# Optimization experiments

Hardware: AMD Instinct MI355X
Metric: run time of the kernel (lower is better)

## Reference

```python
import jax, jax.numpy as jnp
import numpy as np

N, D, H, E = 32768, 1024, 1024, 4


def setup_inputs() -> dict:
    key = jax.random.key(0)
    ks = jax.random.split(key, 10)
    s = 0.02  # xavier-ish init scale for stability
    return {
        "features": jax.random.normal(ks[0], (N, D), dtype=jnp.float32),
        "symbol_ids": jax.random.randint(ks[1], (N,), 0, E, dtype=jnp.int32),
        "W1": jax.random.normal(ks[2], (E, D, H), dtype=jnp.float32) * s,
        "b1": jax.random.normal(ks[3], (E, H), dtype=jnp.float32) * s,
        "W2": jax.random.normal(ks[4], (E, H, H), dtype=jnp.float32) * s,
        "b2": jax.random.normal(ks[5], (E, H), dtype=jnp.float32) * s,
        "W3": jax.random.normal(ks[6], (E, H, 1), dtype=jnp.float32) * s,
        "b3": jax.random.normal(ks[7], (E, 1), dtype=jnp.float32) * s,
        "slope": jax.random.normal(ks[8], (E,), dtype=jnp.float32),
        "intercept": jax.random.normal(ks[9], (E,), dtype=jnp.float32),
    }


def reference(features, symbol_ids, W1, b1, W2, b2, W3, b3, slope, intercept):
    # Run every atom through every expert MLP (E is tiny), then select by symbol.
    # h1: [E, N, H]
    h = jax.nn.relu(jnp.einsum("nd,edh->enh", features, W1) + b1[:, None, :])
    h = jax.nn.relu(jnp.einsum("enh,ehk->enk", h, W2) + b2[:, None, :])
    y = (jnp.einsum("enk,eko->eno", h, W3) + b3[:, None, :])[..., 0]  # [E, N]
    per_atom = slope[:, None] * y + intercept[:, None]                # [E, N]
    sel = symbol_ids[None, :] == jnp.arange(E, dtype=symbol_ids.dtype)[:, None]
    atomic_energies = jnp.sum(jnp.where(sel, per_atom, 0.0), axis=0)  # [N]
    image_energy = jnp.sum(atomic_energies)                           # scalar
    return image_energy
```

## Files before the change

### kernel.cpp

```cpp
#include <hip/hip_runtime.h>
#include <hip/hip_bf16.h>
#include <stdint.h>

#define NATOMS 32768
#define DDIM   1024
#define HDIM   1024
#define ENUM   4
#define MCAP   (NATOMS + ENUM * 128)
#define MTILES 260

typedef unsigned short u16;
typedef unsigned char  u8;
typedef __attribute__((ext_vector_type(8)))  int   i32x8;
typedef __attribute__((ext_vector_type(16))) float f32x16;
typedef __attribute__((ext_vector_type(4)))  float f32x4;

static const size_t XP_OFF   = 0;
static const size_t H1_OFF   = XP_OFF  + (size_t)MCAP * 1024;
static const size_t W1T_OFF  = H1_OFF  + (size_t)MCAP * 1024;
static const size_t W2T_OFF  = W1T_OFF + (size_t)ENUM * 1024 * 1024;
static const size_t PERM_OFF = W2T_OFF + (size_t)ENUM * 1024 * 1024;
static const size_t META_OFF = PERM_OFF + (size_t)MCAP * 4;

__device__ __forceinline__ u8 f2fp8(float x) {
    int w = __builtin_amdgcn_cvt_pk_fp8_f32(x, x, 0, false);
    return (u8)(w & 0xFF);
}

__global__ void k_init(int* __restrict__ perm, int* __restrict__ meta,
                       float* __restrict__ out) {
    int i = blockIdx.x * 256 + threadIdx.x;
    if (i < MCAP) perm[i] = -1;
    if (blockIdx.x == 0) {
        if (threadIdx.x < 256) meta[threadIdx.x] = 0;
        if (threadIdx.x == 0) out[0] = 0.0f;
    }
}

__global__ void k_count(const int* __restrict__ sym, int* __restrict__ meta) {
    int n = blockIdx.x * 256 + threadIdx.x;
    int lane = threadIdx.x & 63;
    int e = sym[n];
#pragma unroll
    for (int j = 0; j < ENUM; ++j) {
        unsigned long long mask = __ballot(e == j);
        if (mask) {
            int leader = __ffsll((long long)mask) - 1;
            if (lane == leader)
                atomicAdd(&meta[j * 16], __popcll(mask));
        }
    }
}

__global__ void k_offsets(int* __restrict__ meta, const float* __restrict__ slope,
                          const float* __restrict__ b3, const float* __restrict__ inter,
                          float* __restrict__ out) {
    if (threadIdx.x == 0 && blockIdx.x == 0) {
        int off = 0;
        float c = 0.f;
        for (int e = 0; e < 4; ++e) {
            meta[128 + e]    = off;
            meta[64 + e*16]  = off;
            int cnt = meta[e * 16];
            c += (float)cnt * (slope[e] * b3[e] + inter[e]);
            off += (cnt + 127) & ~127;
        }
        meta[132] = off;
        out[0] = c;
    }
}

__global__ void k_scatter(const int* __restrict__ sym, int* __restrict__ meta,
                          int* __restrict__ perm) {
    int n = blockIdx.x * 256 + threadIdx.x;
    int lane = threadIdx.x & 63;
    int e = sym[n];
#pragma unroll
    for (int j = 0; j < ENUM; ++j) {
        unsigned long long mask = __ballot(e == j);
        if (mask) {
            int leader = __ffsll((long long)mask) - 1;
            int base = 0;
            if (lane == leader)
                base = atomicAdd(&meta[64 + j * 16], __popcll(mask));
            base = __shfl(base, leader, 64);
            if (e == j) {
                int rank = __popcll(mask & ((1ull << lane) - 1ull));
                perm[base + rank] = n;
            }
        }
    }
}

__global__ void k_convx(const float* __restrict__ F, const int* __restrict__ perm,
                        u8* __restrict__ Xp) {
    int g = blockIdx.x * 256 + threadIdx.x;
    int slot = g >> 7, c = g & 127;
    int src = perm[slot];
    uint2 v;
    if (src < 0) {
        v.x = 0u; v.y = 0u;
    } else {
        const float* fp = F + (size_t)src * 1024 + c * 8;
        int w0 = 0, w1 = 0;
        w0 = __builtin_amdgcn_cvt_pk_fp8_f32(fp[0], fp[1], w0, false);
        w0 = __builtin_amdgcn_cvt_pk_fp8_f32(fp[2], fp[3], w0, true);
        w1 = __builtin_amdgcn_cvt_pk_fp8_f32(fp[4], fp[5], w1, false);
        w1 = __builtin_amdgcn_cvt_pk_fp8_f32(fp[6], fp[7], w1, true);
        v.x = (unsigned)w0; v.y = (unsigned)w1;
    }
    *(uint2*)(void*)(Xp + (size_t)g * 8) = v;
}

__global__ void k_transw(const float* __restrict__ W1, u8* __restrict__ W1T,
                         const float* __restrict__ W2, u8* __restrict__ W2T) {
    __shared__ u8 tile[64][65];
    const float* W  = blockIdx.z ? W2  : W1;
    u8*          WT = blockIdx.z ? W2T : W1T;
    int e  = blockIdx.y;
    int tn = blockIdx.x & 15;
    int tk = blockIdx.x >> 4;
    const float* Wp = W  + (size_t)e * 1024 * 1024;
    u8*         WTp = WT + (size_t)e * 1024 * 1024;
    int c = threadIdx.x & 63, r0 = threadIdx.x >> 6;
#pragma unroll
    for (int i = 0; i < 16; ++i) {
        int r = r0 + i * 4;
        tile[r][c] = f2fp8(32.0f * Wp[(size_t)(tk * 64 + r) * 1024 + tn * 64 + c]);
    }
    __syncthreads();
#pragma unroll
    for (int i = 0; i < 16; ++i) {
        int r = r0 + i * 4;
        WTp[(size_t)(tn * 64 + r) * 1024 + tk * 64 + c] = tile[c][r];
    }
}

template <bool FUSE>
__global__ __launch_bounds__(256, 4)
void k_gemm(const u8* __restrict__ A, const u8* __restrict__ BT,
            const float* __restrict__ bias, u8* __restrict__ C,
            const int* __restrict__ meta, const float* __restrict__ W3,
            const float* __restrict__ slope, float* __restrict__ out) {
    __shared__ u8 As[128 * 128];
    __shared__ u8 Bs[128 * 128];
    const int* offs = meta + 128;

    const int flat = blockIdx.y * 8 + blockIdx.x;
    const int mt = (flat >> 6) * 8 + (flat & 7);
    const int nt = (flat & 63) >> 3;
    if (mt >= MTILES) return;
    const int m0 = mt * 128, n0 = nt * 128;
    int e = (m0 >= offs[1]) + (m0 >= offs[2]) + (m0 >= offs[3]);

    const int t = threadIdx.x;
    const int w = t >> 6, lane = t & 63;
    const int l31 = lane & 31, khalf = lane >> 5;
    const int wm = w & 1, wn = w >> 1;

    const u8* Ag = A + (size_t)m0 * 1024;
    const u8* Bg = BT + (size_t)e * 1024 * 1024 + (size_t)n0 * 1024;

    const int srow   = t >> 3;
    const int gchunk = (t & 7) ^ (srow & 7);

    f32x16 acc[2][2] = {};

    for (int kt = 0; kt < 1024 / 128; ++kt) {
        const int kb = kt * 128;
#pragma unroll
        for (int i = 0; i < 4; ++i) {
            int row = i * 32 + srow;
            __builtin_amdgcn_global_load_lds(
                (const void*)(Ag + (size_t)row * 1024 + kb + gchunk * 16),
                (void*)(As + i * 4096 + w * 1024), 16, 0, 0);
        }
#pragma unroll
        for (int i = 0; i < 4; ++i) {
            int row = i * 32 + srow;
            __builtin_amdgcn_global_load_lds(
                (const void*)(Bg + (size_t)row * 1024 + kb + gchunk * 16),
                (void*)(Bs + i * 4096 + w * 1024), 16, 0, 0);
        }
        __syncthreads();

#pragma unroll
        for (int kk = 0; kk < 2; ++kk) {
            const int c0 = 4 * kk + 2 * khalf;
            i32x8 a[2], b[2];
#pragma unroll
            for (int mi = 0; mi < 2; ++mi) {
                int m = wm * 64 + mi * 32 + l31;
                const u8* base = As + m * 128;
                int lo = ((c0 ^ (m & 7)) << 4);
                uint4 q0 = *(const uint4*)(const void*)(base + lo);
                uint4 q1 = *(const uint4*)(const void*)(base + (lo ^ 16));
                union { uint4 q[2]; i32x8 v; } u;
                u.q[0] = q0; u.q[1] = q1;
                a[mi] = u.v;
            }
#pragma unroll
            for (int ni = 0; ni < 2; ++ni) {
                int n = wn * 64 + ni * 32 + l31;
                const u8* base = Bs + n * 128;
                int lo = ((c0 ^ (n & 7)) << 4);
                uint4 q0 = *(const uint4*)(const void*)(base + lo);
                uint4 q1 = *(const uint4*)(const void*)(base + (lo ^ 16));
                union { uint4 q[2]; i32x8 v; } u;
                u.q[0] = q0; u.q[1] = q1;
                b[ni] = u.v;
            }
#pragma unroll
            for (int mi = 0; mi < 2; ++mi)
#pragma unroll
                for (int ni = 0; ni < 2; ++ni)
                    acc[mi][ni] = __builtin_amdgcn_mfma_scale_f32_32x32x64_f8f6f4(
                        a[mi], b[ni], acc[mi][ni],
                        0, 0,
                        0, 0x7F7F7F7F,
                        0, 0x7A7A7A7A);
        }
        __syncthreads();
    }

    if (!FUSE) {
#pragma unroll
        for (int ni = 0; ni < 2; ++ni) {
            int col = n0 + wn * 64 + ni * 32 + l31;
            float bv = bias[e * 1024 + col];
#pragma unroll
            for (int mi = 0; mi < 2; ++mi) {
                int rowb = m0 + wm * 64 + mi * 32 + 4 * khalf;
#pragma unroll
                for (int reg = 0; reg < 16; ++reg) {
                    int rowg = rowb + (reg & 3) + 8 * (reg >> 2);
                    float v = acc[mi][ni][reg] + bv;
                    v = v > 0.f ? v : 0.f;
                    C[(size_t)rowg * 1024 + col] = f2fp8(v);
                }
            }
        }
    } else {
        const int segEnd = offs[e] + meta[e * 16];
        const float se = slope[e];
        float psum = 0.f;
#pragma unroll
        for (int ni = 0; ni < 2; ++ni) {
            int col = n0 + wn * 64 + ni * 32 + l31;
            float bv  = bias[e * 1024 + col];
            float w3s = W3[e * 1024 + col] * se;
#pragma unroll
            for (int mi = 0; mi < 2; ++mi) {
                int rowb = m0 + wm * 64 + mi * 32 + 4 * khalf;
#pragma unroll
                for (int reg = 0; reg < 16; ++reg) {
                    int rowg = rowb + (reg & 3) + 8 * (reg >> 2);
                    float v = acc[mi][ni][reg] + bv;
                    v = v > 0.f ? v : 0.f;
                    psum += (rowg < segEnd) ? v * w3s : 0.f;
                }
            }
        }
#pragma unroll
        for (int o = 32; o; o >>= 1) psum += __shfl_xor(psum, o, 64);
        float* red = (float*)As;
        if (lane == 0) red[w] = psum;
        __syncthreads();
        if (t == 0) atomicAdd(out, red[0] + red[1] + red[2] + red[3]);
    }
}

extern "C" void kernel_launch(void* const* d_in, const int* in_sizes, int n_in,
                              void* d_out, int out_size, void* d_ws, size_t ws_size,
                              hipStream_t stream) {
    const float* features = (const float*)d_in[0];
    const int*   sym      = (const int*)d_in[1];
    const float* W1       = (const float*)d_in[2];
    const float* b1       = (const float*)d_in[3];
    const float* W2       = (const float*)d_in[4];
    const float* b2       = (const float*)d_in[5];
    const float* W3       = (const float*)d_in[6];
    const float* b3       = (const float*)d_in[7];
    const float* slope    = (const float*)d_in[8];
    const float* inter    = (const float*)d_in[9];
    float* out = (float*)d_out;

    char* ws  = (char*)d_ws;
    u8*  Xp   = (u8*)(ws + XP_OFF);
    u8*  H1b  = (u8*)(ws + H1_OFF);
    u8*  W1T  = (u8*)(ws + W1T_OFF);
    u8*  W2T  = (u8*)(ws + W2T_OFF);
    int* perm = (int*)(ws + PERM_OFF);
    int* meta = (int*)(ws + META_OFF);

    k_init<<<MCAP / 256, 256, 0, stream>>>(perm, meta, out);
    k_count<<<NATOMS / 256, 256, 0, stream>>>(sym, meta);
    k_offsets<<<1, 64, 0, stream>>>(meta, slope, b3, inter, out);
    k_scatter<<<NATOMS / 256, 256, 0, stream>>>(sym, meta, perm);
    k_convx<<<(MCAP * 128) / 256, 256, 0, stream>>>(features, perm, Xp);
    k_transw<<<dim3(256, 4, 2), 256, 0, stream>>>(W1, W1T, W2, W2T);
    k_gemm<false><<<dim3(8, 264), 256, 0, stream>>>(Xp, W1T, b1, H1b, meta,
                                                    nullptr, nullptr, nullptr);
    k_gemm<true><<<dim3(8, 264), 256, 0, stream>>>(H1b, W2T, b2, nullptr, meta,
                                                   W3, slope, out);
}
```

Before: 355.8 us.

## Double-buffer GEMM K-loop with 64-wide tiles and drop init kernel

The GEMM main loop moves from single-buffered 128-wide K tiles to double-buffered 64-wide tiles, so the next tile's global-to-LDS loads are issued while MFMAs run on the current tile. The LDS footprint stays the same. Separately, the init kernel is removed: per-block counts now go to LDS and then to distinct meta slots, k_offsets reduces them, and k_convx checks slot validity from the offsets instead of relying on a -1 perm sentinel. This saves a launch and a global memset, but the loop now has twice as many barriers and the out[0] reset now depends on k_offsets alone.

```diff
diff --git a/kernel.cpp b/kernel.cpp
--- a/kernel.cpp
+++ b/kernel.cpp
@@ -13,7 +13,6 @@
 typedef unsigned char  u8;
 typedef __attribute__((ext_vector_type(8)))  int   i32x8;
 typedef __attribute__((ext_vector_type(16))) float f32x16;
-typedef __attribute__((ext_vector_type(4)))  float f32x4;
 
 static const size_t XP_OFF   = 0;
 static const size_t H1_OFF   = XP_OFF  + (size_t)MCAP * 1024;
@@ -27,41 +26,46 @@
     return (u8)(w & 0xFF);
 }
 
-__global__ void k_init(int* __restrict__ perm, int* __restrict__ meta,
-                       float* __restrict__ out) {
-    int i = blockIdx.x * 256 + threadIdx.x;
-    if (i < MCAP) perm[i] = -1;
-    if (blockIdx.x == 0) {
-        if (threadIdx.x < 256) meta[threadIdx.x] = 0;
-        if (threadIdx.x == 0) out[0] = 0.0f;
-    }
-}
-
 __global__ void k_count(const int* __restrict__ sym, int* __restrict__ meta) {
-    int n = blockIdx.x * 256 + threadIdx.x;
-    int lane = threadIdx.x & 63;
+    __shared__ int cnt[4];
+    int t = threadIdx.x;
+    if (t < 4) cnt[t] = 0;
+    __syncthreads();
+    int n = blockIdx.x * 256 + t;
+    int lane = t & 63;
     int e = sym[n];
 #pragma unroll
     for (int j = 0; j < ENUM; ++j) {
         unsigned long long mask = __ballot(e == j);
         if (mask) {
             int leader = __ffsll((long long)mask) - 1;
-            if (lane == leader)
-                atomicAdd(&meta[j * 16], __popcll(mask));
-        }
-    }
+            if (lane == leader) atomicAdd(&cnt[j], __popcll(mask));
+        }
+    }
+    __syncthreads();
+    if (t < 4) meta[256 + blockIdx.x * 4 + t] = cnt[t];
 }
 
 __global__ void k_offsets(int* __restrict__ meta, const float* __restrict__ slope,
                           const float* __restrict__ b3, const float* __restrict__ inter,
                           float* __restrict__ out) {
-    if (threadIdx.x == 0 && blockIdx.x == 0) {
+    __shared__ int tot[4];
+    int t = threadIdx.x;
+    if (t < 4) {
+        int s = 0;
+#pragma unroll 8
+        for (int b = 0; b < 128; ++b) s += meta[256 + b * 4 + t];
+        tot[t] = s;
+    }
+    __syncthreads();
+    if (t == 0) {
         int off = 0;
         float c = 0.f;
         for (int e = 0; e < 4; ++e) {
+            int cnt = tot[e];
+            meta[e * 16]     = cnt;
             meta[128 + e]    = off;
             meta[64 + e*16]  = off;
-            int cnt = meta[e * 16];
             c += (float)cnt * (slope[e] * b3[e] + inter[e]);
             off += (cnt + 127) & ~127;
         }
@@ -93,14 +97,17 @@
 }
 
 __global__ void k_convx(const float* __restrict__ F, const int* __restrict__ perm,
-                        u8* __restrict__ Xp) {
+                        const int* __restrict__ meta, u8* __restrict__ Xp) {
     int g = blockIdx.x * 256 + threadIdx.x;
     int slot = g >> 7, c = g & 127;
-    int src = perm[slot];
+    const int* offs = meta + 128;
+    int e = (slot >= offs[1]) + (slot >= offs[2]) + (slot >= offs[3]);
+    bool valid = slot < offs[e] + meta[e * 16];
     uint2 v;
-    if (src < 0) {
+    if (!valid) {
         v.x = 0u; v.y = 0u;
     } else {
+        int src = perm[slot];
         const float* fp = F + (size_t)src * 1024 + c * 8;
         int w0 = 0, w1 = 0;
         w0 = __builtin_amdgcn_cvt_pk_fp8_f32(fp[0], fp[1], w0, false);
@@ -142,8 +149,8 @@
             const float* __restrict__ bias, u8* __restrict__ C,
             const int* __restrict__ meta, const float* __restrict__ W3,
             const float* __restrict__ slope, float* __restrict__ out) {
-    __shared__ u8 As[128 * 128];
-    __shared__ u8 Bs[128 * 128];
+    __shared__ u8 As[2][128 * 64];
+    __shared__ u8 Bs[2][128 * 64];
     const int* offs = meta + 128;
 
     const int flat = blockIdx.y * 8 + blockIdx.x;
@@ -161,65 +168,73 @@
     const u8* Ag = A + (size_t)m0 * 1024;
     const u8* Bg = BT + (size_t)e * 1024 * 1024 + (size_t)n0 * 1024;
 
-    const int srow   = t >> 3;
-    const int gchunk = (t & 7) ^ (srow & 7);
+    const int srow   = t >> 2;
+    const int gchunk = (t & 3) ^ (srow & 3);
 
     f32x16 acc[2][2] = {};
 
-    for (int kt = 0; kt < 1024 / 128; ++kt) {
-        const int kb = kt * 128;
-#pragma unroll
-        for (int i = 0; i < 4; ++i) {
-            int row = i * 32 + srow;
-            __builtin_amdgcn_global_load_lds(
-                (const void*)(Ag + (size_t)row * 1024 + kb + gchunk * 16),
-                (void*)(As + i * 4096 + w * 1024), 16, 0, 0);
-        }
-#pragma unroll
-        for (int i = 0; i < 4; ++i) {
-            int row = i * 32 + srow;
-            __builtin_amdgcn_global_load_lds(
-                (const void*)(Bg + (size_t)row * 1024 + kb + gchunk * 16),
-                (void*)(Bs + i * 4096 + w * 1024), 16, 0, 0);
-        }
-        __syncthreads();
-
-#pragma unroll
-        for (int kk = 0; kk < 2; ++kk) {
-            const int c0 = 4 * kk + 2 * khalf;
-            i32x8 a[2], b[2];
-#pragma unroll
-            for (int mi = 0; mi < 2; ++mi) {
-                int m = wm * 64 + mi * 32 + l31;
-                const u8* base = As + m * 128;
-                int lo = ((c0 ^ (m & 7)) << 4);
-                uint4 q0 = *(const uint4*)(const void*)(base + lo);
-                uint4 q1 = *(const uint4*)(const void*)(base + (lo ^ 16));
-                union { uint4 q[2]; i32x8 v; } u;
-                u.q[0] = q0; u.q[1] = q1;
-                a[mi] = u.v;
-            }
-#pragma unroll
-            for (int ni = 0; ni < 2; ++ni) {
-                int n = wn * 64 + ni * 32 + l31;
-                const u8* base = Bs + n * 128;
-                int lo = ((c0 ^ (n & 7)) << 4);
-                uint4 q0 = *(const uint4*)(const void*)(base + lo);
-                uint4 q1 = *(const uint4*)(const void*)(base + (lo ^ 16));
-                union { uint4 q[2]; i32x8 v; } u;
-                u.q[0] = q0; u.q[1] = q1;
-                b[ni] = u.v;
-            }
-#pragma unroll
-            for (int mi = 0; mi < 2; ++mi)
-#pragma unroll
-                for (int ni = 0; ni < 2; ++ni)
-                    acc[mi][ni] = __builtin_amdgcn_mfma_scale_f32_32x32x64_f8f6f4(
-                        a[mi], b[ni], acc[mi][ni],
-                        0, 0,
-                        0, 0x7F7F7F7F,
-                        0, 0x7A7A7A7A);
-        }
+#pragma unroll
+    for (int i = 0; i < 2; ++i)
+        __builtin_amdgcn_global_load_lds(
+            (const void*)(Ag + (size_t)(i * 64 + srow) * 1024 + gchunk * 16),
+            (void*)(As[0] + i * 4096 + w * 1024), 16, 0, 0);
+#pragma unroll
+    for (int i = 0; i < 2; ++i)
+        __builtin_amdgcn_global_load_lds(
+            (const void*)(Bg + (size_t)(i * 64 + srow) * 1024 + gchunk * 16),
+            (void*)(Bs[0] + i * 4096 + w * 1024), 16, 0, 0);
+    __syncthreads();
+
+    for (int kt = 0; kt < 16; ++kt) {
+        const int cur = kt & 1;
+        if (kt < 15) {
+            const int kb = (kt + 1) * 64;
+            const int nxt = cur ^ 1;
+#pragma unroll
+            for (int i = 0; i < 2; ++i)
+                __builtin_amdgcn_global_load_lds(
+                    (const void*)(Ag + (size_t)(i * 64 + srow) * 1024 + kb + gchunk * 16),
+                    (void*)(As[nxt] + i * 4096 + w * 1024), 16, 0, 0);
+#pragma unroll
+            for (int i = 0; i < 2; ++i)
+                __builtin_amdgcn_global_load_lds(
+                    (const void*)(Bg + (size_t)(i * 64 + srow) * 1024 + kb + gchunk * 16),
+                    (void*)(Bs[nxt] + i * 4096 + w * 1024), 16, 0, 0);
+        }
+
+        const int c0 = 2 * khalf;
+        i32x8 a[2], b[2];
+#pragma unroll
+        for (int mi = 0; mi < 2; ++mi) {
+            int m = wm * 64 + mi * 32 + l31;
+            const u8* base = As[cur] + m * 64;
+            int lo = ((c0 ^ (m & 3)) << 4);
+            uint4 q0 = *(const uint4*)(const void*)(base + lo);
+            uint4 q1 = *(const uint4*)(const void*)(base + (lo ^ 16));
+            union { uint4 q[2]; i32x8 v; } u;
+            u.q[0] = q0; u.q[1] = q1;
+            a[mi] = u.v;
+        }
+#pragma unroll
+        for (int ni = 0; ni < 2; ++ni) {
+            int n = wn * 64 + ni * 32 + l31;
+            const u8* base = Bs[cur] + n * 64;
+            int lo = ((c0 ^ (n & 3)) << 4);
+            uint4 q0 = *(const uint4*)(const void*)(base + lo);
+            uint4 q1 = *(const uint4*)(const void*)(base + (lo ^ 16));
+            union { uint4 q[2]; i32x8 v; } u;
+            u.q[0] = q0; u.q[1] = q1;
+            b[ni] = u.v;
+        }
+#pragma unroll
+        for (int mi = 0; mi < 2; ++mi)
+#pragma unroll
+            for (int ni = 0; ni < 2; ++ni)
+                acc[mi][ni] = __builtin_amdgcn_mfma_scale_f32_32x32x64_f8f6f4(
+                    a[mi], b[ni], acc[mi][ni],
+                    0, 0,
+                    0, 0x7F7F7F7F,
+                    0, 0x7A7A7A7A);
         __syncthreads();
     }
 
@@ -263,7 +278,7 @@
         }
 #pragma unroll
         for (int o = 32; o; o >>= 1) psum += __shfl_xor(psum, o, 64);
-        float* red = (float*)As;
+        float* red = (float*)As[0];
         if (lane == 0) red[w] = psum;
         __syncthreads();
         if (t == 0) atomicAdd(out, red[0] + red[1] + red[2] + red[3]);
@@ -293,11 +308,10 @@
     int* perm = (int*)(ws + PERM_OFF);
     int* meta = (int*)(ws + META_OFF);
 
-    k_init<<<MCAP / 256, 256, 0, stream>>>(perm, meta, out);
     k_count<<<NATOMS / 256, 256, 0, stream>>>(sym, meta);
-    k_offsets<<<1, 64, 0, stream>>>(meta, slope, b3, inter, out);
+    k_offsets<<<1, 256, 0, stream>>>(meta, slope, b3, inter, out);
     k_scatter<<<NATOMS / 256, 256, 0, stream>>>(sym, meta, perm);
-    k_convx<<<(MCAP * 128) / 256, 256, 0, stream>>>(features, perm, Xp);
+    k_convx<<<(MCAP * 128) / 256, 256, 0, stream>>>(features, perm, meta, Xp);
     k_transw<<<dim3(256, 4, 2), 256, 0, stream>>>(W1, W1T, W2, W2T);
     k_gemm<false><<<dim3(8, 264), 256, 0, stream>>>(Xp, W1T, b1, H1b, meta,
                                                     nullptr, nullptr, nullptr);
```

Measured after the change: 374.6 us. 1.05x slower.
